# Performance work log

Measured on AMD Instinct MI355X. Metric: run time of the kernel, lower is better.

Reference implementation:

```python
import jax, jax.numpy as jnp
import numpy as np

B, S, H, E, V = 128, 400, 256, 128, 50000
PAD = 250  # extended-vocab padding hard-coded in the torch module


def setup_inputs() -> dict:
    key = jax.random.key(0)
    ks = jax.random.split(key, 20)
    return {
        "input_token": jax.random.randint(ks[0], (B, 1), 0, V),
        "last_decoder_hidden": jax.random.normal(ks[1], (B, H), jnp.float32),
        "encoder_states": jax.random.normal(ks[2], (B, S, H), jnp.float32),
        "full_input_var": jax.random.randint(ks[3], (B, S), 0, V + PAD),
        "emb_table": jax.random.normal(ks[4], (V, E), jnp.float32) * 0.02,
        "gru_w_ih": jax.random.normal(ks[5], (3 * H, E), jnp.float32) * 0.05,
        "gru_w_hh": jax.random.normal(ks[6], (3 * H, H), jnp.float32) * 0.05,
        "gru_b_ih": jax.random.normal(ks[7], (3 * H,), jnp.float32) * 0.05,
        "gru_b_hh": jax.random.normal(ks[8], (3 * H,), jnp.float32) * 0.05,
        "w_h": jax.random.normal(ks[9], (H,), jnp.float32),
        "w_s": jax.random.normal(ks[10], (H,), jnp.float32),
        "att_bias": jax.random.normal(ks[11], (1,), jnp.float32),
        "attn_v": jax.random.normal(ks[12], (H,), jnp.float32),
        "gen_w": jax.random.normal(ks[13], (1, 2 * H + E), jnp.float32) * 0.05,
        "gen_b": jax.random.normal(ks[14], (1,), jnp.float32) * 0.05,
        "outh_w": jax.random.normal(ks[15], (E, 2 * H), jnp.float32) * 0.05,
        "outh_b": jax.random.normal(ks[16], (E,), jnp.float32) * 0.05,
        "outv_w": jax.random.normal(ks[17], (V, E), jnp.float32) * 0.05,
        "outv_b": jax.random.normal(ks[18], (V,), jnp.float32) * 0.05,
    }


def reference(input_token, last_decoder_hidden, encoder_states, full_input_var,
              emb_table, gru_w_ih, gru_w_hh, gru_b_ih, gru_b_hh,
              w_h, w_s, att_bias, attn_v, gen_w, gen_b,
              outh_w, outh_b, outv_w, outv_b):
    b, s, h = encoder_states.shape
    v = outv_w.shape[0]
    # Embedding lookup (dropout is identity in eval mode): [B, E]
    x = emb_table[input_token[:, 0]]
    # Single-step GRU cell (PyTorch gate order: r, z, n)
    gi = x @ gru_w_ih.T + gru_b_ih
    gh = last_decoder_hidden @ gru_w_hh.T + gru_b_hh
    i_r, i_z, i_n = jnp.split(gi, 3, axis=-1)
    h_r, h_z, h_n = jnp.split(gh, 3, axis=-1)
    r = jax.nn.sigmoid(i_r + h_r)
    z = jax.nn.sigmoid(i_z + h_z)
    n = jnp.tanh(i_n + r * h_n)
    h_new = (1.0 - z) * n + z * last_decoder_hidden  # [B, H]
    # Bahdanau-style elementwise attention
    att = jnp.tanh(w_h * encoder_states + w_s * h_new[:, None, :] + att_bias)  # [B,S,H]
    scores = jnp.einsum('bsh,h->bs', att, attn_v)
    att_dist = jax.nn.softmax(scores, axis=-1)  # [B, S]
    context = jnp.einsum('bs,bsh->bh', att_dist, encoder_states)  # [B, H]
    dec_ctx = jnp.concatenate([h_new, context], axis=-1)  # [B, 2H]
    p_vocab = jax.nn.softmax((dec_ctx @ outh_w.T + outh_b) @ outv_w.T + outv_b, axis=-1)  # [B, V]
    p_gen = jax.nn.sigmoid(jnp.concatenate([dec_ctx, x], axis=1) @ gen_w.T + gen_b)  # [B, 1]
    # Pointer scatter-add into extended vocab [B, V+PAD]
    rows = jnp.arange(b)[:, None]
    token_input_dist = jnp.zeros((b, v + PAD), p_vocab.dtype).at[rows, full_input_var].add(att_dist)
    p_final = jnp.concatenate([p_vocab * p_gen, jnp.zeros((b, PAD), p_vocab.dtype)], axis=1) \
              + (1.0 - p_gen) * token_input_dist
    return (h_new, p_final, p_gen, p_vocab, att_dist)
```

## Files before the change

### kernel.cpp

```cpp
#include <hip/hip_runtime.h>
#include <hip/hip_bf16.h>


#define B_ 128
#define S_ 400
#define H_ 256
#define E_ 128
#define V_ 50000
#define PAD_ 250
#define VP_ (V_ + PAD_)
#define NSUM_ 16

typedef unsigned short ushort_t;
typedef __attribute__((ext_vector_type(8))) short bf16x8;
typedef __attribute__((ext_vector_type(4))) float f32x4;

__device__ __forceinline__ unsigned short f2bfu(float f) {
    __hip_bfloat16 h = __float2bfloat16(f);
    union { __hip_bfloat16 h; unsigned short u; } c;
    c.h = h;
    return c.u;
}

__device__ __forceinline__ float sigmoid_fast(float x) {
    return 1.0f / (1.0f + __expf(-x));
}

__device__ __forceinline__ float tanh_fast(float x) {
    return 1.0f - 2.0f / (__expf(2.0f * x) + 1.0f);
}

__device__ __forceinline__ float waveReduceSumAll(float v) {
#pragma unroll
    for (int off = 1; off < 64; off <<= 1) v += __shfl_xor(v, off, 64);
    return v;
}

#define XH_PITCH 392
__global__ __launch_bounds__(256) void k_gates(
    const int* __restrict__ token, const float* __restrict__ emb,
    const float* __restrict__ hprev,
    const float* __restrict__ w_ih, const float* __restrict__ w_hh,
    float* __restrict__ gi_ws, float* __restrict__ gh_ws) {
    __shared__ ushort_t xh[B_ * XH_PITCH];
    __shared__ int toks[B_];
    int t = threadIdx.x;
    if (t < B_) toks[t] = token[t];
    __syncthreads();
#pragma unroll
    for (int i = 0; i < 16; i++) {
        int fidx = i * 256 + t;
        int b = fidx >> 5, k4 = fidx & 31;
        float4 q = *(const float4*)(emb + (size_t)toks[b] * E_ + k4 * 4);
        ushort4 u;
        u.x = f2bfu(q.x); u.y = f2bfu(q.y); u.z = f2bfu(q.z); u.w = f2bfu(q.w);
        *(ushort4*)&xh[b * XH_PITCH + k4 * 4] = u;
    }
#pragma unroll
    for (int i = 0; i < 32; i++) {
        int fidx = i * 256 + t;
        int b = fidx >> 6, k4 = fidx & 63;
        float4 q = *(const float4*)(hprev + (size_t)b * H_ + k4 * 4);
        ushort4 u;
        u.x = f2bfu(q.x); u.y = f2bfu(q.y); u.z = f2bfu(q.z); u.w = f2bfu(q.w);
        *(ushort4*)&xh[b * XH_PITCH + 128 + k4 * 4] = u;
    }
    __syncthreads();

    int wave = t >> 6, lane = t & 63, lm = lane & 15, quad = lane >> 4;
    int vt = blockIdx.x * 4 + wave;
    bool isIH = vt < 48;
    int n0 = (isIH ? vt : vt - 48) * 16;
    const float* wbase = isIH ? w_ih : w_hh;
    int K = isIH ? E_ : H_;
    int aoff = isIH ? 0 : 128;
    float* gout = isIH ? gi_ws : gh_ws;
    int v = n0 + lm;
    const float* wrow = wbase + (size_t)v * K;

    f32x4 acc[8];
#pragma unroll
    for (int bt = 0; bt < 8; bt++) acc[bt] = (f32x4){0.f, 0.f, 0.f, 0.f};

    for (int kc = 0; kc < (K >> 5); kc++) {
        int k0 = kc * 32 + quad * 8;
        float4 w0 = *(const float4*)(wrow + k0);
        float4 w1 = *(const float4*)(wrow + k0 + 4);
        bf16x8 bf;
        bf[0] = (short)f2bfu(w0.x); bf[1] = (short)f2bfu(w0.y);
        bf[2] = (short)f2bfu(w0.z); bf[3] = (short)f2bfu(w0.w);
        bf[4] = (short)f2bfu(w1.x); bf[5] = (short)f2bfu(w1.y);
        bf[6] = (short)f2bfu(w1.z); bf[7] = (short)f2bfu(w1.w);
#pragma unroll
        for (int bt = 0; bt < 8; bt++) {
            bf16x8 af = *(const bf16x8*)&xh[(bt * 16 + lm) * XH_PITCH + aoff + k0];
            acc[bt] = __builtin_amdgcn_mfma_f32_16x16x32_bf16(af, bf, acc[bt], 0, 0, 0);
        }
    }
#pragma unroll
    for (int bt = 0; bt < 8; bt++)
#pragma unroll
        for (int r = 0; r < 4; r++) {
            int b = bt * 16 + quad * 4 + r;
            gout[(size_t)b * 768 + v] = acc[bt][r];
        }
}

__global__ __launch_bounds__(1024) void k_mega(
    const float* __restrict__ gi_ws, const float* __restrict__ gh_ws,
    const float* __restrict__ b_ih, const float* __restrict__ b_hh,
    const float* __restrict__ hprev,
    const int* __restrict__ token, const float* __restrict__ emb,
    const float* __restrict__ enc,
    const float* __restrict__ w_h, const float* __restrict__ w_s,
    const float* __restrict__ att_bias, const float* __restrict__ attn_v,
    const float* __restrict__ outh_w, const float* __restrict__ outh_b,
    const float* __restrict__ gen_w, const float* __restrict__ gen_b,
    float* __restrict__ out_hnew, float* __restrict__ out_attd,
    float* __restrict__ out_pgen,
    float* __restrict__ attd_ws, float* __restrict__ hidden_ws,
    float* __restrict__ pgen_ws, float* __restrict__ row_sum16) {
    int b = blockIdx.x;
    int t = threadIdx.x;
    int wave = t >> 6, lane = t & 63;
    __shared__ float hn_s[H_], whs[H_], vs[H_], cs[H_];
    __shared__ float sc[S_];
    __shared__ float cmerge[H_];
    __shared__ float mred[16], lred[16];
    __shared__ float dc[2 * H_ + E_];
    __shared__ float r2[16];

    if (b == 0) {
        for (int i = t; i < NSUM_ * B_; i += 1024) row_sum16[i] = 0.0f;
    }
    if (t < H_) {
        float ir = gi_ws[(size_t)b * 768 + t] + b_ih[t];
        float iz = gi_ws[(size_t)b * 768 + 256 + t] + b_ih[256 + t];
        float in_ = gi_ws[(size_t)b * 768 + 512 + t] + b_ih[512 + t];
        float hr = gh_ws[(size_t)b * 768 + t] + b_hh[t];
        float hz = gh_ws[(size_t)b * 768 + 256 + t] + b_hh[256 + t];
        float hn = gh_ws[(size_t)b * 768 + 512 + t] + b_hh[512 + t];
        float hp = hprev[(size_t)b * H_ + t];
        float r = sigmoid_fast(ir + hr);
        float z = sigmoid_fast(iz + hz);
        float n = tanh_fast(in_ + r * hn);
        float h = (1.0f - z) * n + z * hp;
        hn_s[t] = h;
        out_hnew[(size_t)b * H_ + t] = h;
        whs[t] = w_h[t];
        vs[t] = attn_v[t];
        cs[t] = w_s[t] * h + att_bias[0];
        cmerge[t] = 0.0f;
    }
    __syncthreads();

    int h0 = lane * 4;
    float m_w = -1e30f, l_w = 0.0f;
    float cx0 = 0.f, cx1 = 0.f, cx2 = 0.f, cx3 = 0.f;
    for (int s = wave; s < S_; s += 16) {
        float4 u = *(const float4*)(enc + ((size_t)(b * S_ + s)) * H_ + h0);
        float p = vs[h0 + 0] * tanh_fast(whs[h0 + 0] * u.x + cs[h0 + 0])
                + vs[h0 + 1] * tanh_fast(whs[h0 + 1] * u.y + cs[h0 + 1])
                + vs[h0 + 2] * tanh_fast(whs[h0 + 2] * u.z + cs[h0 + 2])
                + vs[h0 + 3] * tanh_fast(whs[h0 + 3] * u.w + cs[h0 + 3]);
        p = waveReduceSumAll(p);
        if (lane == 0) sc[s] = p;
        float mn = fmaxf(m_w, p);
        float scale = __expf(m_w - mn);
        float w = __expf(p - mn);
        cx0 = cx0 * scale + w * u.x;
        cx1 = cx1 * scale + w * u.y;
        cx2 = cx2 * scale + w * u.z;
        cx3 = cx3 * scale + w * u.w;
        l_w = l_w * scale + w;
        m_w = mn;
    }
    if (lane == 0) mred[wave] = m_w;
    __syncthreads();

    float M = -1e30f;
#pragma unroll
    for (int wv = 0; wv < 16; wv++) M = fmaxf(M, mred[wv]);
    float wf = __expf(m_w - M);
    if (lane == 0) lred[wave] = l_w * wf;
    atomicAdd(&cmerge[h0 + 0], cx0 * wf);
    atomicAdd(&cmerge[h0 + 1], cx1 * wf);
    atomicAdd(&cmerge[h0 + 2], cx2 * wf);
    atomicAdd(&cmerge[h0 + 3], cx3 * wf);
    __syncthreads();
    float L = 0.0f;
#pragma unroll
    for (int wv = 0; wv < 16; wv++) L += lred[wv];
    float invL = 1.0f / L;

    if (t < S_) {
        float a = __expf(sc[t] - M) * invL;
        attd_ws[b * S_ + t] = a;
        out_attd[(size_t)b * S_ + t] = a;
    }
    if (t < H_) {
        dc[t] = hn_s[t];
        dc[H_ + t] = cmerge[t] * invL;
    }
    if (t < E_) dc[2 * H_ + t] = emb[(size_t)token[b] * E_ + t];
    __syncthreads();

    {
        int r = t >> 3, sub = t & 7;
        const float* wrow = outh_w + (size_t)r * (2 * H_);
        float acc = 0.0f;
#pragma unroll
        for (int i = 0; i < 16; i++) {
            int k = i * 32 + sub * 4;
            float4 q = *(const float4*)(wrow + k);
            acc += dc[k] * q.x + dc[k + 1] * q.y + dc[k + 2] * q.z + dc[k + 3] * q.w;
        }
        acc += __shfl_down(acc, 4, 64);
        acc += __shfl_down(acc, 2, 64);
        acc += __shfl_down(acc, 1, 64);
        if (sub == 0) hidden_ws[(size_t)b * E_ + r] = acc + outh_b[r];
    }
    float pp = (t < 2 * H_ + E_) ? dc[t] * gen_w[t] : 0.0f;
    pp = waveReduceSumAll(pp);
    if (lane == 0) r2[wave] = pp;
    __syncthreads();
    if (t == 0) {
        float g = 0.0f;
#pragma unroll
        for (int wv = 0; wv < 16; wv++) g += r2[wv];
        g = sigmoid_fast(g + gen_b[0]);
        pgen_ws[b] = g;
        out_pgen[b] = g;
    }
}

#define VT_TOTAL (V_ / 16)
#define HID_PITCH 136
__global__ __launch_bounds__(256) void k_vocab_mfma(
    const float* __restrict__ outv_w, const float* __restrict__ outv_b,
    const float* __restrict__ hidden_ws,
    float* __restrict__ out_pvocab, float* __restrict__ row_sum16) {
    __shared__ ushort_t hid[B_ * HID_PITCH];
    __shared__ float rsum[B_];
    int t = threadIdx.x;

    const float4* h4 = (const float4*)hidden_ws;
#pragma unroll
    for (int i = 0; i < 16; i++) {
        int fidx = i * 256 + t;
        float4 q = h4[fidx];
        int row = fidx >> 5;
        int col = (fidx & 31) << 2;
        ushort4 u;
        u.x = f2bfu(q.x); u.y = f2bfu(q.y); u.z = f2bfu(q.z); u.w = f2bfu(q.w);
        *(ushort4*)&hid[row * HID_PITCH + col] = u;
    }
    if (t < B_) rsum[t] = 0.0f;
    __syncthreads();

    int wave = t >> 6, lane = t & 63, lm = lane & 15, quad = lane >> 4;
    int vt = blockIdx.x * 4 + wave;

    if (vt < VT_TOTAL) {
        int v = vt * 16 + lm;
        const float* wrow = outv_w + (size_t)v * E_;

        f32x4 acc[8];
#pragma unroll
        for (int bt = 0; bt < 8; bt++) acc[bt] = (f32x4){0.f, 0.f, 0.f, 0.f};

#pragma unroll
        for (int kc = 0; kc < 4; kc++) {
            int k0 = kc * 32 + quad * 8;
            float4 w0 = *(const float4*)(wrow + k0);
            float4 w1 = *(const float4*)(wrow + k0 + 4);
            bf16x8 bf;
            bf[0] = (short)f2bfu(w0.x); bf[1] = (short)f2bfu(w0.y);
            bf[2] = (short)f2bfu(w0.z); bf[3] = (short)f2bfu(w0.w);
            bf[4] = (short)f2bfu(w1.x); bf[5] = (short)f2bfu(w1.y);
            bf[6] = (short)f2bfu(w1.z); bf[7] = (short)f2bfu(w1.w);
#pragma unroll
            for (int bt = 0; bt < 8; bt++) {
                bf16x8 af = *(const bf16x8*)&hid[(bt * 16 + lm) * HID_PITCH + k0];
                acc[bt] = __builtin_amdgcn_mfma_f32_16x16x32_bf16(af, bf, acc[bt], 0, 0, 0);
            }
        }

        float bias = outv_b[v];
#pragma unroll
        for (int bt = 0; bt < 8; bt++) {
#pragma unroll
            for (int r = 0; r < 4; r++) {
                int b = bt * 16 + quad * 4 + r;
                float e = __expf(fminf(acc[bt][r] + bias, 60.0f));
                out_pvocab[(size_t)b * V_ + v] = e;
                float s = e;
                s += __shfl_xor(s, 1);
                s += __shfl_xor(s, 2);
                s += __shfl_xor(s, 4);
                s += __shfl_xor(s, 8);
                if (lm == 0) atomicAdd(&rsum[b], s);
            }
        }
    }
    __syncthreads();
    if (t < B_) atomicAdd(&row_sum16[(blockIdx.x & (NSUM_ - 1)) * B_ + t], rsum[t]);
}

__global__ __launch_bounds__(256) void k_final(
    const float* __restrict__ row_sum16, const float* __restrict__ pgen_ws,
    float* __restrict__ out_pfinal, float* __restrict__ out_pvocab) {
    int b = blockIdx.y;
    int jbase = blockIdx.x * 2048;
    int t = threadIdx.x;
    float rs = 0.0f;
#pragma unroll
    for (int i = 0; i < NSUM_; i++) rs += row_sum16[i * B_ + b];
    float inv = 1.0f / rs;
    float pg = pgen_ws[b];
#pragma unroll
    for (int i = 0; i < 8; i++) {
        int j = jbase + i * 256 + t;
        if (j < VP_) {
            if (j < V_) {
                float p = out_pvocab[(size_t)b * V_ + j] * inv;
                out_pvocab[(size_t)b * V_ + j] = p;
                out_pfinal[(size_t)b * VP_ + j] = p * pg;
            } else {
                out_pfinal[(size_t)b * VP_ + j] = 0.0f;
            }
        }
    }
}

__global__ __launch_bounds__(256) void k_scatter(
    const int* __restrict__ fiv, const float* __restrict__ attd_ws,
    const float* __restrict__ pgen_ws, float* __restrict__ out_pfinal) {
    int b = blockIdx.x;
    int t = threadIdx.x;
    float omg = 1.0f - pgen_ws[b];
    for (int s = t; s < S_; s += 256) {
        int idx = fiv[b * S_ + s];
        float val = omg * attd_ws[b * S_ + s];
        atomicAdd(&out_pfinal[(size_t)b * VP_ + idx], val);
    }
}

extern "C" void kernel_launch(void* const* d_in, const int* in_sizes, int n_in,
                              void* d_out, int out_size, void* d_ws, size_t ws_size,
                              hipStream_t stream) {
    const int* token = (const int*)d_in[0];
    const float* hprev = (const float*)d_in[1];
    const float* enc = (const float*)d_in[2];
    const int* fiv = (const int*)d_in[3];
    const float* emb = (const float*)d_in[4];
    const float* w_ih = (const float*)d_in[5];
    const float* w_hh = (const float*)d_in[6];
    const float* b_ih = (const float*)d_in[7];
    const float* b_hh = (const float*)d_in[8];
    const float* w_h = (const float*)d_in[9];
    const float* w_s = (const float*)d_in[10];
    const float* att_bias = (const float*)d_in[11];
    const float* attn_v = (const float*)d_in[12];
    const float* gen_w = (const float*)d_in[13];
    const float* gen_b = (const float*)d_in[14];
    const float* outh_w = (const float*)d_in[15];
    const float* outh_b = (const float*)d_in[16];
    const float* outv_w = (const float*)d_in[17];
    const float* outv_b = (const float*)d_in[18];

    float* out = (float*)d_out;
    float* out_hnew = out;
    float* out_pfinal = out + (size_t)B_ * H_;
    float* out_pgen = out_pfinal + (size_t)B_ * VP_;
    float* out_pvocab = out_pgen + B_;
    float* out_attd = out_pvocab + (size_t)B_ * V_;

    float* wsf = (float*)d_ws;
    float* gi_ws = wsf;
    float* gh_ws = wsf + 98304;
    float* attd_ws = wsf + 196608;
    float* hidden_ws = wsf + 247808;
    float* pgen_ws = wsf + 264192;
    float* row_sum16 = wsf + 264320;

    k_gates<<<24, 256, 0, stream>>>(token, emb, hprev, w_ih, w_hh, gi_ws, gh_ws);
    k_mega<<<B_, 1024, 0, stream>>>(gi_ws, gh_ws, b_ih, b_hh, hprev, token, emb,
                                    enc, w_h, w_s, att_bias, attn_v,
                                    outh_w, outh_b, gen_w, gen_b,
                                    out_hnew, out_attd, out_pgen,
                                    attd_ws, hidden_ws, pgen_ws, row_sum16);
    k_vocab_mfma<<<782, 256, 0, stream>>>(outv_w, outv_b, hidden_ws, out_pvocab, row_sum16);
    k_final<<<dim3(25, B_), 256, 0, stream>>>(row_sum16, pgen_ws, out_pfinal, out_pvocab);
    k_scatter<<<B_, 256, 0, stream>>>(fiv, attd_ws, pgen_ws, out_pfinal);
}
```

Measured before the change: 233.1 us.

## Split attention across sequence chunks with a separate combine kernel

The single per-batch attention kernel becomes a split-S kernel: 8 chunks per batch row, each with 256 threads, computing partial max, sum and context. A new combine kernel merges these partials with log-sum-exp rescaling and then runs the projection and gate work. The aim is to spread the encoder-state reads over more blocks than 128 for better occupancy. The cost is an extra launch, workspace traffic for the partials, and the GRU cell being recomputed in every chunk; k_gates also now gives each block a smaller shared tile holding only x or only h.

```diff
diff --git a/kernel.cpp b/kernel.cpp
--- a/kernel.cpp
+++ b/kernel.cpp
@@ -9,6 +9,8 @@
 #define V_ 50000
 #define PAD_ 250
 #define VP_ (V_ + PAD_)
+#define NC_ 8
+#define CS_ (S_ / NC_)
 #define NSUM_ 16
 
 typedef unsigned short ushort_t;
@@ -36,47 +38,47 @@
     return v;
 }
 
-#define XH_PITCH 392
 __global__ __launch_bounds__(256) void k_gates(
     const int* __restrict__ token, const float* __restrict__ emb,
     const float* __restrict__ hprev,
     const float* __restrict__ w_ih, const float* __restrict__ w_hh,
     float* __restrict__ gi_ws, float* __restrict__ gh_ws) {
-    __shared__ ushort_t xh[B_ * XH_PITCH];
+    __shared__ ushort_t xh[B_ * 264];
     __shared__ int toks[B_];
     int t = threadIdx.x;
-    if (t < B_) toks[t] = token[t];
-    __syncthreads();
-#pragma unroll
-    for (int i = 0; i < 16; i++) {
-        int fidx = i * 256 + t;
-        int b = fidx >> 5, k4 = fidx & 31;
-        float4 q = *(const float4*)(emb + (size_t)toks[b] * E_ + k4 * 4);
-        ushort4 u;
-        u.x = f2bfu(q.x); u.y = f2bfu(q.y); u.z = f2bfu(q.z); u.w = f2bfu(q.w);
-        *(ushort4*)&xh[b * XH_PITCH + k4 * 4] = u;
-    }
-#pragma unroll
-    for (int i = 0; i < 32; i++) {
-        int fidx = i * 256 + t;
-        int b = fidx >> 6, k4 = fidx & 63;
-        float4 q = *(const float4*)(hprev + (size_t)b * H_ + k4 * 4);
-        ushort4 u;
-        u.x = f2bfu(q.x); u.y = f2bfu(q.y); u.z = f2bfu(q.z); u.w = f2bfu(q.w);
-        *(ushort4*)&xh[b * XH_PITCH + 128 + k4 * 4] = u;
+    bool isIH = blockIdx.x < 12;
+    if (isIH) {
+        if (t < B_) toks[t] = token[t];
+        __syncthreads();
+#pragma unroll
+        for (int i = 0; i < 16; i++) {
+            int fidx = i * 256 + t;
+            int b = fidx >> 5, k4 = fidx & 31;
+            float4 q = *(const float4*)(emb + (size_t)toks[b] * E_ + k4 * 4);
+            ushort4 u;
+            u.x = f2bfu(q.x); u.y = f2bfu(q.y); u.z = f2bfu(q.z); u.w = f2bfu(q.w);
+            *(ushort4*)&xh[b * 136 + k4 * 4] = u;
+        }
+    } else {
+#pragma unroll
+        for (int i = 0; i < 32; i++) {
+            int fidx = i * 256 + t;
+            int b = fidx >> 6, k4 = fidx & 63;
+            float4 q = *(const float4*)(hprev + (size_t)b * H_ + k4 * 4);
+            ushort4 u;
+            u.x = f2bfu(q.x); u.y = f2bfu(q.y); u.z = f2bfu(q.z); u.w = f2bfu(q.w);
+            *(ushort4*)&xh[b * 264 + k4 * 4] = u;
+        }
     }
     __syncthreads();
 
     int wave = t >> 6, lane = t & 63, lm = lane & 15, quad = lane >> 4;
-    int vt = blockIdx.x * 4 + wave;
-    bool isIH = vt < 48;
-    int n0 = (isIH ? vt : vt - 48) * 16;
-    const float* wbase = isIH ? w_ih : w_hh;
+    int tile = (isIH ? blockIdx.x : blockIdx.x - 12) * 4 + wave;
+    int v = tile * 16 + lm;
     int K = isIH ? E_ : H_;
-    int aoff = isIH ? 0 : 128;
+    int pitch = isIH ? 136 : 264;
+    const float* wrow = (isIH ? w_ih : w_hh) + (size_t)v * K;
     float* gout = isIH ? gi_ws : gh_ws;
-    int v = n0 + lm;
-    const float* wrow = wbase + (size_t)v * K;
 
     f32x4 acc[8];
 #pragma unroll
@@ -93,7 +95,7 @@
         bf[6] = (short)f2bfu(w1.z); bf[7] = (short)f2bfu(w1.w);
 #pragma unroll
         for (int bt = 0; bt < 8; bt++) {
-            bf16x8 af = *(const bf16x8*)&xh[(bt * 16 + lm) * XH_PITCH + aoff + k0];
+            bf16x8 af = *(const bf16x8*)&xh[(bt * 16 + lm) * pitch + k0];
             acc[bt] = __builtin_amdgcn_mfma_f32_16x16x32_bf16(af, bf, acc[bt], 0, 0, 0);
         }
     }
@@ -106,34 +108,22 @@
         }
 }
 
-__global__ __launch_bounds__(1024) void k_mega(
+__global__ __launch_bounds__(256) void k_attn(
     const float* __restrict__ gi_ws, const float* __restrict__ gh_ws,
     const float* __restrict__ b_ih, const float* __restrict__ b_hh,
     const float* __restrict__ hprev,
-    const int* __restrict__ token, const float* __restrict__ emb,
     const float* __restrict__ enc,
     const float* __restrict__ w_h, const float* __restrict__ w_s,
     const float* __restrict__ att_bias, const float* __restrict__ attn_v,
-    const float* __restrict__ outh_w, const float* __restrict__ outh_b,
-    const float* __restrict__ gen_w, const float* __restrict__ gen_b,
-    float* __restrict__ out_hnew, float* __restrict__ out_attd,
-    float* __restrict__ out_pgen,
-    float* __restrict__ attd_ws, float* __restrict__ hidden_ws,
-    float* __restrict__ pgen_ws, float* __restrict__ row_sum16) {
-    int b = blockIdx.x;
+    float* __restrict__ out_hnew,
+    float* __restrict__ sc_ws, float* __restrict__ ml_ws, float* __restrict__ ctxp_ws) {
+    int c = blockIdx.x, b = blockIdx.y;
     int t = threadIdx.x;
     int wave = t >> 6, lane = t & 63;
-    __shared__ float hn_s[H_], whs[H_], vs[H_], cs[H_];
-    __shared__ float sc[S_];
-    __shared__ float cmerge[H_];
-    __shared__ float mred[16], lred[16];
-    __shared__ float dc[2 * H_ + E_];
-    __shared__ float r2[16];
-
-    if (b == 0) {
-        for (int i = t; i < NSUM_ * B_; i += 1024) row_sum16[i] = 0.0f;
-    }
-    if (t < H_) {
+    __shared__ float whs[H_], vs[H_], cs[H_], cmerge[H_];
+    __shared__ float mred[4], lred[4];
+
+    {
         float ir = gi_ws[(size_t)b * 768 + t] + b_ih[t];
         float iz = gi_ws[(size_t)b * 768 + 256 + t] + b_ih[256 + t];
         float in_ = gi_ws[(size_t)b * 768 + 512 + t] + b_ih[512 + t];
@@ -145,8 +135,7 @@
         float z = sigmoid_fast(iz + hz);
         float n = tanh_fast(in_ + r * hn);
         float h = (1.0f - z) * n + z * hp;
-        hn_s[t] = h;
-        out_hnew[(size_t)b * H_ + t] = h;
+        if (c == 0) out_hnew[(size_t)b * H_ + t] = h;
         whs[t] = w_h[t];
         vs[t] = attn_v[t];
         cs[t] = w_s[t] * h + att_bias[0];
@@ -157,14 +146,15 @@
     int h0 = lane * 4;
     float m_w = -1e30f, l_w = 0.0f;
     float cx0 = 0.f, cx1 = 0.f, cx2 = 0.f, cx3 = 0.f;
-    for (int s = wave; s < S_; s += 16) {
+    for (int si = wave; si < CS_; si += 4) {
+        int s = c * CS_ + si;
         float4 u = *(const float4*)(enc + ((size_t)(b * S_ + s)) * H_ + h0);
         float p = vs[h0 + 0] * tanh_fast(whs[h0 + 0] * u.x + cs[h0 + 0])
                 + vs[h0 + 1] * tanh_fast(whs[h0 + 1] * u.y + cs[h0 + 1])
                 + vs[h0 + 2] * tanh_fast(whs[h0 + 2] * u.z + cs[h0 + 2])
                 + vs[h0 + 3] * tanh_fast(whs[h0 + 3] * u.w + cs[h0 + 3]);
         p = waveReduceSumAll(p);
-        if (lane == 0) sc[s] = p;
+        if (lane == 0) sc_ws[b * S_ + s] = p;
         float mn = fmaxf(m_w, p);
         float scale = __expf(m_w - mn);
         float w = __expf(p - mn);
@@ -177,30 +167,63 @@
     }
     if (lane == 0) mred[wave] = m_w;
     __syncthreads();
-
-    float M = -1e30f;
-#pragma unroll
-    for (int wv = 0; wv < 16; wv++) M = fmaxf(M, mred[wv]);
-    float wf = __expf(m_w - M);
+    float m_c = fmaxf(fmaxf(mred[0], mred[1]), fmaxf(mred[2], mred[3]));
+    float wf = __expf(m_w - m_c);
     if (lane == 0) lred[wave] = l_w * wf;
     atomicAdd(&cmerge[h0 + 0], cx0 * wf);
     atomicAdd(&cmerge[h0 + 1], cx1 * wf);
     atomicAdd(&cmerge[h0 + 2], cx2 * wf);
     atomicAdd(&cmerge[h0 + 3], cx3 * wf);
     __syncthreads();
+    if (t == 0) {
+        ml_ws[(b * NC_ + c) * 2 + 0] = m_c;
+        ml_ws[(b * NC_ + c) * 2 + 1] = lred[0] + lred[1] + lred[2] + lred[3];
+    }
+    ctxp_ws[(size_t)(b * NC_ + c) * H_ + t] = cmerge[t];
+}
+
+__global__ __launch_bounds__(1024) void k_combine(
+    const float* __restrict__ sc_ws, const float* __restrict__ ml_ws,
+    const float* __restrict__ ctxp_ws,
+    const float* __restrict__ out_hnew,
+    const int* __restrict__ token, const float* __restrict__ emb,
+    const float* __restrict__ outh_w, const float* __restrict__ outh_b,
+    const float* __restrict__ gen_w, const float* __restrict__ gen_b,
+    float* __restrict__ out_attd, float* __restrict__ out_pgen,
+    float* __restrict__ attd_ws, float* __restrict__ hidden_ws,
+    float* __restrict__ pgen_ws, float* __restrict__ row_sum16) {
+    int b = blockIdx.x;
+    int t = threadIdx.x;
+    int wave = t >> 6, lane = t & 63;
+    __shared__ float ml[NC_ * 2];
+    __shared__ float dc[2 * H_ + E_];
+    __shared__ float r2[16];
+
+    if (b == 0) {
+        for (int i = t; i < NSUM_ * B_; i += 1024) row_sum16[i] = 0.0f;
+    }
+    if (t < NC_ * 2) ml[t] = ml_ws[b * NC_ * 2 + t];
+    __syncthreads();
+    float M = -1e30f;
+#pragma unroll
+    for (int c = 0; c < NC_; c++) M = fmaxf(M, ml[2 * c]);
     float L = 0.0f;
 #pragma unroll
-    for (int wv = 0; wv < 16; wv++) L += lred[wv];
+    for (int c = 0; c < NC_; c++) L += ml[2 * c + 1] * __expf(ml[2 * c] - M);
     float invL = 1.0f / L;
 
     if (t < S_) {
-        float a = __expf(sc[t] - M) * invL;
+        float a = __expf(sc_ws[b * S_ + t] - M) * invL;
         attd_ws[b * S_ + t] = a;
         out_attd[(size_t)b * S_ + t] = a;
     }
     if (t < H_) {
-        dc[t] = hn_s[t];
-        dc[H_ + t] = cmerge[t] * invL;
+        float acc = 0.0f;
+#pragma unroll
+        for (int c = 0; c < NC_; c++)
+            acc += __expf(ml[2 * c] - M) * ctxp_ws[(size_t)(b * NC_ + c) * H_ + t];
+        dc[t] = out_hnew[(size_t)b * H_ + t];
+        dc[H_ + t] = acc * invL;
     }
     if (t < E_) dc[2 * H_ + t] = emb[(size_t)token[b] * E_ + t];
     __syncthreads();
@@ -383,13 +406,18 @@
     float* hidden_ws = wsf + 247808;
     float* pgen_ws = wsf + 264192;
     float* row_sum16 = wsf + 264320;
+    float* sc_ws = wsf + 266368;
+    float* ml_ws = wsf + 317568;
+    float* ctxp_ws = wsf + 319616;
 
     k_gates<<<24, 256, 0, stream>>>(token, emb, hprev, w_ih, w_hh, gi_ws, gh_ws);
-    k_mega<<<B_, 1024, 0, stream>>>(gi_ws, gh_ws, b_ih, b_hh, hprev, token, emb,
-                                    enc, w_h, w_s, att_bias, attn_v,
-                                    outh_w, outh_b, gen_w, gen_b,
-                                    out_hnew, out_attd, out_pgen,
-                                    attd_ws, hidden_ws, pgen_ws, row_sum16);
+    k_attn<<<dim3(NC_, B_), 256, 0, stream>>>(gi_ws, gh_ws, b_ih, b_hh, hprev,
+                                              enc, w_h, w_s, att_bias, attn_v,
+                                              out_hnew, sc_ws, ml_ws, ctxp_ws);
+    k_combine<<<B_, 1024, 0, stream>>>(sc_ws, ml_ws, ctxp_ws, out_hnew, token, emb,
+                                       outh_w, outh_b, gen_w, gen_b,
+                                       out_attd, out_pgen,
+                                       attd_ws, hidden_ws, pgen_ws, row_sum16);
     k_vocab_mfma<<<782, 256, 0, stream>>>(outv_w, outv_b, hidden_ws, out_pvocab, row_sum16);
     k_final<<<dim3(25, B_), 256, 0, stream>>>(row_sum16, pgen_ws, out_pfinal, out_pvocab);
     k_scatter<<<B_, 256, 0, stream>>>(fiv, attd_ws, pgen_ws, out_pfinal);
```

Result: faster. 225.7 us (-3.2%).
